# Kernel optimization log

Hardware: AMD Instinct MI355X
Metric: run time of the kernel (lower is better)

The kernel has to match this reference:

```python
import jax, jax.numpy as jnp
import numpy as np

DIMS = [2048, 1024, 512, 256, 128, 64, 32, 16, 8, 4, 2]
IN_CH = [3, 8, 32, 64, 64, 64, 128, 256, 512, 512, 512]
FEAT = [8, 32, 64, 64, 64, 128, 256, 512, 512, 512, 1024]
B = 512
K = 16


def setup_inputs() -> dict:
    key = jax.random.key(0)
    keys = jax.random.split(key, 64)
    inp = {"x": jax.random.normal(keys[0], (B, 3, 2048), dtype=jnp.float32)}
    for i, d in enumerate(DIMS):
        inp[f"c{i}"] = jax.random.randint(keys[1 + i], (d,), 0, 3, dtype=jnp.int64)
    for i in range(11):
        cin, f = IN_CH[i], FEAT[i]
        inp[f"W{i+1}"] = jax.random.normal(keys[20 + 2 * i], (3 * f, cin), dtype=jnp.float32) / jnp.sqrt(jnp.float32(cin))
        inp[f"b{i+1}"] = jnp.zeros((3 * f,), dtype=jnp.float32)
    inp["Wfc"] = jax.random.normal(keys[60], (K, 1024), dtype=jnp.float32) / jnp.sqrt(jnp.float32(1024))
    inp["bfc"] = jnp.zeros((K,), dtype=jnp.float32)
    return inp


def _kdconv(x, W, b, sel, featdim, dim):
    # pointwise conv (kernel size 1) + relu: [B, in, dim] -> [B, 3*featdim, dim]
    y = jax.nn.relu(jnp.einsum('oi,bid->bod', W, x) + b[None, :, None])
    bsz = y.shape[0]
    # faithful to torch: view [B, featdim, 3*dim], then gather index d*3 + sel[d]
    y = y.reshape(bsz, featdim, 3 * dim)
    idx = sel + 3 * jnp.arange(dim, dtype=sel.dtype)
    y = jnp.take(y, idx, axis=2)                       # [B, featdim, dim]
    y = y.reshape(bsz, featdim, dim // 2, 2)
    return jnp.max(y, axis=-1)                          # [B, featdim, dim//2]


def reference(x, c0, c1, c2, c3, c4, c5, c6, c7, c8, c9, c10,
              W1, b1, W2, b2, W3, b3, W4, b4, W5, b5, W6, b6,
              W7, b7, W8, b8, W9, b9, W10, b10, W11, b11, Wfc, bfc):
    cs = [c0, c1, c2, c3, c4, c5, c6, c7, c8, c9, c10]
    Ws = [W1, W2, W3, W4, W5, W6, W7, W8, W9, W10, W11]
    bs = [b1, b2, b3, b4, b5, b6, b7, b8, b9, b10, b11]
    y = x
    for i in range(11):
        y = _kdconv(y, Ws[i], bs[i], cs[i], FEAT[i], DIMS[i])
    y = y.reshape(-1, 1024)
    logits = y @ Wfc.T + bfc
    return jax.nn.log_softmax(logits, axis=1)
```

## Files before the change

### kernel.cpp

```cpp
#include <hip/hip_runtime.h>
#include <cstdint>
#include <cmath>


typedef __attribute__((ext_vector_type(8))) short bhalf8;
typedef __attribute__((ext_vector_type(4))) float floatx4;

__device__ __forceinline__ unsigned short f2bf(float f) {
    uint32_t u = __float_as_uint(f);
    u += 0x7FFFu + ((u >> 16) & 1u);
    return (unsigned short)(u >> 16);
}
__device__ __forceinline__ float bf2f(unsigned short u) {
    return __uint_as_float(((uint32_t)u) << 16);
}

struct WPrep {
    const float* src[9];
    unsigned short* dst[9];
    int n4[9];
};

__global__ __launch_bounds__(256)
void l01_kernel(const float* __restrict__ x,
                const float* __restrict__ W0, const float* __restrict__ b0,
                const int* __restrict__ sel0,
                const float* __restrict__ W1, const float* __restrict__ b1,
                const int* __restrict__ sel1,
                unsigned short* __restrict__ out,
                WPrep wp, int nL1) {
    const int tid = threadIdx.x;

    if ((int)blockIdx.x >= nL1) {
        const int stride = (gridDim.x - nL1) * 256;
        const int g0 = (blockIdx.x - nL1) * 256 + tid;
        #pragma unroll
        for (int l = 0; l < 9; ++l) {
            const float4* s = reinterpret_cast<const float4*>(wp.src[l]);
            uint2* d = reinterpret_cast<uint2*>(wp.dst[l]);
            for (int i = g0; i < wp.n4[l]; i += stride) {
                const float4 v = s[i];
                uint2 o;
                o.x = (uint32_t)f2bf(v.x) | ((uint32_t)f2bf(v.y) << 16);
                o.y = (uint32_t)f2bf(v.z) | ((uint32_t)f2bf(v.w) << 16);
                d[i] = o;
            }
        }
        return;
    }

    __shared__ float W0s[24][3]; __shared__ float b0s[24];
    __shared__ float W1s[96][8]; __shared__ float b1s[96];
    if (tid < 24) {
        W0s[tid][0] = W0[tid * 3 + 0];
        W0s[tid][1] = W0[tid * 3 + 1];
        W0s[tid][2] = W0[tid * 3 + 2];
        b0s[tid] = b0[tid];
    }
    if (tid < 96) {
        #pragma unroll
        for (int k = 0; k < 8; ++k) W1s[tid][k] = W1[tid * 8 + k];
        b1s[tid] = b1[tid];
    }
    __syncthreads();

    const int gid = blockIdx.x * 256 + tid;
    const int b  = gid >> 9;
    const int j1 = gid & 511;
    const float* xb = x + (size_t)b * 3 * 2048;

    float cols[2][8];
    int q1v[2];
    #pragma unroll
    for (int pos1 = 0; pos1 < 2; ++pos1) {
        const int d1 = 2 * j1 + pos1;
        const int e1 = 3 * d1 + sel1[d1];
        const int q1 = (e1 >= 1024) + (e1 >= 2048);
        const int p1 = e1 - q1 * 1024;
        q1v[pos1] = q1;

        float xv[2][3]; int qq0[2];
        #pragma unroll
        for (int pos0 = 0; pos0 < 2; ++pos0) {
            const int d0 = 2 * p1 + pos0;
            const int e0 = 3 * d0 + sel0[d0];
            const int q0 = (e0 >= 2048) + (e0 >= 4096);
            const int p0 = e0 - q0 * 2048;
            qq0[pos0] = q0;
            xv[pos0][0] = xb[p0];
            xv[pos0][1] = xb[2048 + p0];
            xv[pos0][2] = xb[4096 + p0];
        }
        #pragma unroll
        for (int f = 0; f < 8; ++f) {
            const int r0 = 3 * f + qq0[0], r1 = 3 * f + qq0[1];
            const float v0 = b0s[r0] + W0s[r0][0]*xv[0][0] + W0s[r0][1]*xv[0][1] + W0s[r0][2]*xv[0][2];
            const float v1 = b0s[r1] + W0s[r1][0]*xv[1][0] + W0s[r1][1]*xv[1][1] + W0s[r1][2]*xv[1][2];
            cols[pos1][f] = fmaxf(fmaxf(v0, v1), 0.f);
        }
    }

    unsigned short o[32];
    #pragma unroll
    for (int f = 0; f < 32; ++f) {
        const int r0 = 3 * f + q1v[0], r1 = 3 * f + q1v[1];
        float v0 = b1s[r0], v1 = b1s[r1];
        #pragma unroll
        for (int k = 0; k < 8; ++k) {
            v0 = fmaf(cols[0][k], W1s[r0][k], v0);
            v1 = fmaf(cols[1][k], W1s[r1][k], v1);
        }
        o[f] = f2bf(fmaxf(fmaxf(v0, v1), 0.f));
    }
    bhalf8* op = reinterpret_cast<bhalf8*>(out + (size_t)gid * 32);
    #pragma unroll
    for (int i = 0; i < 4; ++i) {
        bhalf8 v;
        #pragma unroll
        for (int k = 0; k < 8; ++k) v[k] = (short)o[8*i + k];
        op[i] = v;
    }
}


template<int RB>
__device__ __forceinline__ int swaddr(int row, int colbyte) {
    constexpr int SM = (RB / 16 >= 8) ? 7 : (RB / 16 - 1);
    return row * RB + (colbyte ^ ((row & SM) << 4));
}

template<int CIN>
__device__ __forceinline__ int wswz(int i) {
    constexpr int GPR = CIN / 8;
    constexpr int RB  = CIN * 2;
    const int row = i / GPR, c = i - row * GPR;
    return swaddr<RB>(row, c * 16);
}

template<int DIM, int CIN, int FEAT>
__device__ __forceinline__ void kdlayer(char* pool, int offIn, int offOut,
                                        int qpOff, int offW,
                                        const float* __restrict__ bg, int tid) {
    constexpr int NH  = CIN / 32;
    constexpr int MT  = DIM / 16;
    constexpr int NT  = FEAT / 16;
    constexpr int RBW = CIN * 2;
    constexpr int RBO = FEAT * 2;
    constexpr int WM  = (MT < 8) ? MT : 8;
    constexpr int WN  = 8 / WM;
    constexpr int MPW = MT / WM;
    constexpr int NPW = NT / WN;

    const unsigned short* qp = (const unsigned short*)(pool + qpOff);
    const int wv = tid >> 6, ln = tid & 63;
    const int g = ln >> 4, l15 = ln & 15;
    const int wm = wv % WM, wn = wv / WM;

    bhalf8 aC[MPW][NH];
    uint32_t qpk[MPW];
    #pragma unroll
    for (int i = 0; i < MPW; ++i) {
        const int mt = wm + i * WM;
        const int pa = qp[mt * 16 + l15] & 0xFFF;
        #pragma unroll
        for (int ks = 0; ks < NH; ++ks)
            aC[i][ks] = *(const bhalf8*)(pool + offIn +
                          swaddr<RBW>(pa, (ks * 32 + g * 8) * 2));
        const ushort4 qq = *(const ushort4*)(qp + mt * 16 + g * 4);
        qpk[i] = (uint32_t)(qq.x >> 12) | ((uint32_t)(qq.y >> 12) << 4)
               | ((uint32_t)(qq.z >> 12) << 8) | ((uint32_t)(qq.w >> 12) << 12);
    }

    #pragma unroll
    for (int ntj = 0; ntj < NPW; ++ntj) {
        const int nt = wn * NPW + ntj;
        const int f = nt * 16 + l15;
        bhalf8 bF[3][NH];
        #pragma unroll
        for (int q = 0; q < 3; ++q)
            #pragma unroll
            for (int ks = 0; ks < NH; ++ks)
                bF[q][ks] = *(const bhalf8*)(pool + offW +
                              swaddr<RBW>(3 * f + q, (ks * 32 + g * 8) * 2));
        const float bv0 = bg[3 * f + 0];
        const float bv1 = bg[3 * f + 1];
        const float bv2 = bg[3 * f + 2];
        #pragma unroll
        for (int i = 0; i < MPW; ++i) {
            floatx4 a0 = (floatx4){0.f,0.f,0.f,0.f};
            floatx4 a1 = (floatx4){0.f,0.f,0.f,0.f};
            floatx4 a2 = (floatx4){0.f,0.f,0.f,0.f};
            #pragma unroll
            for (int ks = 0; ks < NH; ++ks) {
                a0 = __builtin_amdgcn_mfma_f32_16x16x32_bf16(aC[i][ks], bF[0][ks], a0, 0, 0, 0);
                a1 = __builtin_amdgcn_mfma_f32_16x16x32_bf16(aC[i][ks], bF[1][ks], a1, 0, 0, 0);
                a2 = __builtin_amdgcn_mfma_f32_16x16x32_bf16(aC[i][ks], bF[2][ks], a2, 0, 0, 0);
            }
            const int mt = wm + i * WM;
            const int j0 = mt * 8 + g * 2;
            float v[4];
            #pragma unroll
            for (int r = 0; r < 4; ++r) {
                const int qi = (qpk[i] >> (4 * r)) & 0xF;
                const float pre = (qi == 0) ? a0[r] : (qi == 1 ? a1[r] : a2[r]);
                const float bq  = (qi == 0) ? bv0  : (qi == 1 ? bv1  : bv2);
                v[r] = pre + bq;
            }
            *(unsigned short*)(pool + offOut + swaddr<RBO>(j0,     f * 2)) =
                f2bf(fmaxf(fmaxf(v[0], v[1]), 0.f));
            *(unsigned short*)(pool + offOut + swaddr<RBO>(j0 + 1, f * 2)) =
                f2bf(fmaxf(fmaxf(v[2], v[3]), 0.f));
        }
    }
}

__global__ __launch_bounds__(512, 4)
void chain_kernel(const unsigned short* __restrict__ act,
                  unsigned short* __restrict__ out,
                  const unsigned short* __restrict__ w2, const float* __restrict__ b2, const int* __restrict__ s2,
                  const unsigned short* __restrict__ w3, const float* __restrict__ b3, const int* __restrict__ s3,
                  const unsigned short* __restrict__ w4, const float* __restrict__ b4, const int* __restrict__ s4,
                  const unsigned short* __restrict__ w5, const float* __restrict__ b5, const int* __restrict__ s5) {
    __shared__ __align__(16) char pool[79872];
    const int tid = threadIdx.x;
    const int b = blockIdx.x;

    bhalf8 w3r[3];
    #pragma unroll
    for (int u = 0; u < 3; ++u)
        w3r[u] = ((const bhalf8*)w3)[u * 512 + tid];

    {
        unsigned short* qp2 = (unsigned short*)(pool + 0);
        unsigned short* qp3 = (unsigned short*)(pool + 1024);
        unsigned short* qp4 = (unsigned short*)(pool + 1536);
        unsigned short* qp5 = (unsigned short*)(pool + 1792);
        { const int d = tid;
          const int e = 3 * d + s2[d];
          const int q = (e >= 512) + (e >= 1024);
          qp2[d] = (unsigned short)((q << 12) | (e - q * 512)); }
        if (tid < 256) { const int d = tid;
          const int e = 3 * d + s3[d];
          const int q = (e >= 256) + (e >= 512);
          qp3[d] = (unsigned short)((q << 12) | (e - q * 256)); }
        if (tid < 128) { const int d = tid;
          const int e = 3 * d + s4[d];
          const int q = (e >= 128) + (e >= 256);
          qp4[d] = (unsigned short)((q << 12) | (e - q * 128)); }
        if (tid < 64)  { const int d = tid;
          const int e = 3 * d + s5[d];
          const int q = (e >= 64) + (e >= 128);
          qp5[d] = (unsigned short)((q << 12) | (e - q * 64)); }
    }

    {
        const bhalf8* src = (const bhalf8*)(act + (size_t)b * 512 * 32);
        bhalf8 inr[4];
        #pragma unroll
        for (int k = 0; k < 4; ++k) inr[k] = src[k * 512 + tid];
        const bhalf8* ws = (const bhalf8*)w2;
        bhalf8 w2r[2];
        w2r[0] = ws[tid];
        if (tid < 256) w2r[1] = ws[512 + tid];
        #pragma unroll
        for (int k = 0; k < 4; ++k)
            *(bhalf8*)(pool + 2048 + wswz<32>(k * 512 + tid)) = inr[k];
        *(bhalf8*)(pool + 34816 + wswz<32>(tid)) = w2r[0];
        if (tid < 256)
            *(bhalf8*)(pool + 34816 + wswz<32>(512 + tid)) = w2r[1];
    }
    __syncthreads();

    kdlayer<512, 32, 64>(pool, 2048, 47104, 0, 34816, b2, tid);
    __syncthreads();

    bhalf8 w4r[3];
    #pragma unroll
    for (int u = 0; u < 3; ++u)
        w4r[u] = ((const bhalf8*)w4)[u * 512 + tid];
    #pragma unroll
    for (int u = 0; u < 3; ++u)
        *(bhalf8*)(pool + 2048 + wswz<64>(u * 512 + tid)) = w3r[u];
    __syncthreads();

    kdlayer<256, 64, 64>(pool, 47104, 26624, 1024, 2048, b3, tid);
    __syncthreads();

    bhalf8 w5r[6];
    #pragma unroll
    for (int u = 0; u < 6; ++u)
        w5r[u] = ((const bhalf8*)w5)[u * 512 + tid];
    #pragma unroll
    for (int u = 0; u < 3; ++u)
        *(bhalf8*)(pool + 47104 + wswz<64>(u * 512 + tid)) = w4r[u];
    __syncthreads();

    kdlayer<128, 64, 64>(pool, 26624, 71680, 1536, 47104, b4, tid);
    __syncthreads();

    #pragma unroll
    for (int u = 0; u < 6; ++u)
        *(bhalf8*)(pool + 2048 + wswz<64>(u * 512 + tid)) = w5r[u];
    __syncthreads();

    kdlayer<64, 64, 128>(pool, 71680, 51200, 1792, 2048, b5, tid);
    __syncthreads();

    {
        char* dst = (char*)(out + (size_t)b * 32 * 128);
        const int off = tid * 16;
        const bhalf8 v = *(const bhalf8*)(pool + 51200 +
                                          swaddr<256>(off >> 8, off & 255));
        *(bhalf8*)(dst + off) = v;
    }
}

template<int CIN, int BT>
__global__ __launch_bounds__(256)
void kdmfma_kernel(const unsigned short* __restrict__ act,
                   const unsigned short* __restrict__ Wq,
                   const float* __restrict__ bias,
                   const int*   __restrict__ sel,
                   unsigned short* __restrict__ out,
                   int feat, int dim, int nbt) {
    constexpr int KS  = (CIN >= 128) ? 128 : CIN;
    constexpr int NH  = KS / 32;
    constexpr int LDK = KS + 8;
    constexpr int TPA = 256 / BT;
    constexpr int EA  = KS / TPA;
    constexpr int NSA = EA / 8;
    constexpr int NSW = KS / 32;
    constexpr int MF  = 2;
    constexpr int NF  = (BT == 64) ? 2 : 1;
    __shared__ __align__(16) unsigned short Ab[BT][LDK];
    __shared__ __align__(16) unsigned short Wb[64][LDK];

    const int dimh = dim >> 1;
    const int bt = blockIdx.x % nbt;
    const int j  = blockIdx.x / nbt;
    const int f0 = blockIdx.y * 64;
    const int b0 = bt * BT;

    const int tid  = threadIdx.x;
    const int lane = tid & 63;
    const int wave = tid >> 6;

    const int srowA = tid / TPA;
    const int kgA   = (tid % TPA) * EA;
    const int srowW = tid >> 2;
    const int kgW   = (tid & 3) * (KS / 4);

    const int rowBase = (BT == 64) ? (wave & 1) * 32 : 0;
    const int colBase = (BT == 64) ? (wave >> 1) * 32 : wave * 16;

    floatx4 acc[2][MF][NF];
    #pragma unroll
    for (int pp = 0; pp < 2; ++pp)
        #pragma unroll
        for (int mi = 0; mi < MF; ++mi)
            #pragma unroll
            for (int ni = 0; ni < NF; ++ni)
                acc[pp][mi][ni] = (floatx4){0.f, 0.f, 0.f, 0.f};
    int qv[2];

    #pragma unroll
    for (int pp = 0; pp < 2; ++pp) {
        const int d = 2 * j + pp;
        const int s = sel[d];
        const int e = 3 * d + s;
        const int q = (e >= dim) + (e >= 2 * dim);
        const int p = e - q * dim;
        qv[pp] = q;

        const unsigned short* Ap = act + ((size_t)(b0 + srowA) * dim + p) * CIN + kgA;
        const unsigned short* Wp = Wq + ((size_t)(3 * (f0 + srowW) + q)) * CIN + kgW;

        bhalf8 pa[NSA], pw[NSW];
        #pragma unroll
        for (int u = 0; u < NSA; ++u)
            pa[u] = *reinterpret_cast<const bhalf8*>(Ap + u * 8);
        #pragma unroll
        for (int u = 0; u < NSW; ++u)
            pw[u] = *reinterpret_cast<const bhalf8*>(Wp + u * 8);

        for (int k0 = 0; k0 < CIN; k0 += KS) {
            __syncthreads();
            #pragma unroll
            for (int u = 0; u < NSA; ++u)
                *reinterpret_cast<bhalf8*>(&Ab[srowA][kgA + u * 8]) = pa[u];
            #pragma unroll
            for (int u = 0; u < NSW; ++u)
                *reinterpret_cast<bhalf8*>(&Wb[srowW][kgW + u * 8]) = pw[u];
            if (k0 + KS < CIN) {
                #pragma unroll
                for (int u = 0; u < NSA; ++u)
                    pa[u] = *reinterpret_cast<const bhalf8*>(Ap + k0 + KS + u * 8);
                #pragma unroll
                for (int u = 0; u < NSW; ++u)
                    pw[u] = *reinterpret_cast<const bhalf8*>(Wp + k0 + KS + u * 8);
            }
            __syncthreads();

            #pragma unroll
            for (int ks = 0; ks < NH; ++ks) {
                const int kk = ks * 32 + (lane >> 4) * 8;
                bhalf8 aF[MF], bF[NF];
                #pragma unroll
                for (int mi = 0; mi < MF; ++mi)
                    aF[mi] = *reinterpret_cast<const bhalf8*>(
                        &Ab[rowBase + mi * 16 + (lane & 15)][kk]);
                #pragma unroll
                for (int ni = 0; ni < NF; ++ni)
                    bF[ni] = *reinterpret_cast<const bhalf8*>(
                        &Wb[colBase + ni * 16 + (lane & 15)][kk]);
                #pragma unroll
                for (int mi = 0; mi < MF; ++mi)
                    #pragma unroll
                    for (int ni = 0; ni < NF; ++ni)
                        acc[pp][mi][ni] = __builtin_amdgcn_mfma_f32_16x16x32_bf16(
                            aF[mi], bF[ni], acc[pp][mi][ni], 0, 0, 0);
            }
        }
    }

    const int orow = (lane >> 4) << 2;
    const int ocol = lane & 15;
    #pragma unroll
    for (int mi = 0; mi < MF; ++mi)
        #pragma unroll
        for (int ni = 0; ni < NF; ++ni) {
            const int fc = f0 + colBase + ni * 16 + ocol;
            const float bv0 = bias[3 * fc + qv[0]];
            const float bv1 = bias[3 * fc + qv[1]];
            #pragma unroll
            for (int i = 0; i < 4; ++i) {
                const int br = b0 + rowBase + mi * 16 + orow + i;
                const float v = fmaxf(fmaxf(acc[0][mi][ni][i] + bv0,
                                            acc[1][mi][ni][i] + bv1), 0.f);
                out[((size_t)br * dimh + j) * feat + fc] = f2bf(v);
            }
        }
}

__global__ __launch_bounds__(256)
void fc_lsm_kernel(const unsigned short* __restrict__ y,
                   const float* __restrict__ Wfc,
                   const float* __restrict__ bfc,
                   float* __restrict__ out) {
    const int b   = blockIdx.x;
    const int tid = threadIdx.x;
    __shared__ __align__(16) float ys[1024];
    __shared__ float lg[16];

    {
        const ushort4 v = reinterpret_cast<const ushort4*>(y + (size_t)b * 1024)[tid];
        ys[tid * 4 + 0] = bf2f(v.x);
        ys[tid * 4 + 1] = bf2f(v.y);
        ys[tid * 4 + 2] = bf2f(v.z);
        ys[tid * 4 + 3] = bf2f(v.w);
    }
    __syncthreads();

    const int l = tid >> 4, lane = tid & 15;
    const float4* w4 = reinterpret_cast<const float4*>(Wfc + (size_t)l * 1024);
    const float4* y4 = reinterpret_cast<const float4*>(ys);
    float p = 0.f;
    #pragma unroll
    for (int i = 0; i < 16; ++i) {
        const float4 a = y4[lane + 16 * i];
        const float4 w = w4[lane + 16 * i];
        p += a.x * w.x + a.y * w.y + a.z * w.z + a.w * w.w;
    }
    #pragma unroll
    for (int off = 8; off > 0; off >>= 1) p += __shfl_down(p, off, 16);
    if (lane == 0) lg[l] = p + bfc[l];
    __syncthreads();

    if (tid < 16) {
        float m = -1e30f;
        #pragma unroll
        for (int i = 0; i < 16; ++i) m = fmaxf(m, lg[i]);
        float s = 0.f;
        #pragma unroll
        for (int i = 0; i < 16; ++i) s += expf(lg[i] - m);
        out[b * 16 + tid] = lg[tid] - m - logf(s);
    }
}

extern "C" void kernel_launch(void* const* d_in, const int* in_sizes, int n_in,
                              void* d_out, int out_size, void* d_ws, size_t ws_size,
                              hipStream_t stream) {
    static const int LFEAT[11] = {8, 32, 64, 64, 64, 128, 256, 512, 512, 512, 1024};
    static const int LDIM[11]  = {2048, 1024, 512, 256, 128, 64, 32, 16, 8, 4, 2};
    static const int LCIN[11]  = {3, 8, 32, 64, 64, 64, 128, 256, 512, 512, 512};

    const float* x = (const float*)d_in[0];
    const int B = in_sizes[0] / (3 * 2048);

    const size_t slot = (size_t)B * 32 * 512;
    float* bufA = (float*)d_ws;
    float* bufB = bufA + slot;
    unsigned short* wq = (unsigned short*)(bufB + slot);

    const float* W[11]; const float* bi[11]; const int* sl[11];
    for (int i = 0; i < 11; ++i) {
        W[i]  = (const float*)d_in[12 + 2 * i];
        bi[i] = (const float*)d_in[13 + 2 * i];
        sl[i] = (const int*)d_in[1 + i];
    }

    unsigned short* wqp[11];
    {
        size_t off = 0;
        for (int i = 2; i <= 10; ++i) {
            wqp[i] = wq + off;
            off += (size_t)3 * LFEAT[i] * LCIN[i];
        }
    }

    unsigned short* actA = (unsigned short*)bufA;
    unsigned short* actB = (unsigned short*)bufB;

    {
        WPrep wp;
        for (int i = 2; i <= 10; ++i) {
            wp.src[i - 2] = W[i];
            wp.dst[i - 2] = wqp[i];
            wp.n4[i - 2]  = (3 * LFEAT[i] * LCIN[i]) / 4;
        }
        const int nL1 = (B * 512) / 256;
        l01_kernel<<<nL1 + 768, 256, 0, stream>>>(x, W[0], bi[0], sl[0],
                                                  W[1], bi[1], sl[1],
                                                  actB, wp, nL1);
    }

    chain_kernel<<<B, 512, 0, stream>>>(actB, actA,
                                        wqp[2], bi[2], sl[2],
                                        wqp[3], bi[3], sl[3],
                                        wqp[4], bi[4], sl[4],
                                        wqp[5], bi[5], sl[5]);

    const int nbt64 = B / 64;
    const int nbt32 = B / 32;

    {   dim3 g((LDIM[6]/2) * nbt64, LFEAT[6]/64);
        kdmfma_kernel<128, 64><<<g, 256, 0, stream>>>(actA, wqp[6], bi[6], sl[6], actB, LFEAT[6], LDIM[6], nbt64); }
    {   dim3 g((LDIM[7]/2) * nbt64, LFEAT[7]/64);
        kdmfma_kernel<256, 64><<<g, 256, 0, stream>>>(actB, wqp[7], bi[7], sl[7], actA, LFEAT[7], LDIM[7], nbt64); }

    {   dim3 g((LDIM[8]/2) * nbt32, LFEAT[8]/64);
        kdmfma_kernel<512, 32><<<g, 256, 0, stream>>>(actA, wqp[8], bi[8], sl[8], actB, LFEAT[8], LDIM[8], nbt32); }
    {   dim3 g((LDIM[9]/2) * nbt32, LFEAT[9]/64);
        kdmfma_kernel<512, 32><<<g, 256, 0, stream>>>(actB, wqp[9], bi[9], sl[9], actA, LFEAT[9], LDIM[9], nbt32); }
    {   dim3 g((LDIM[10]/2) * nbt32, LFEAT[10]/64);
        kdmfma_kernel<512, 32><<<g, 256, 0, stream>>>(actA, wqp[10], bi[10], sl[10], actB, LFEAT[10], LDIM[10], nbt32); }

    fc_lsm_kernel<<<B, 256, 0, stream>>>(actB, (const float*)d_in[34],
                                         (const float*)d_in[35], (float*)d_out);
}
```

Before: 85.29 us.

## Fuse layers 0-1 into chain kernel, split weight prep, add kdmfma2 for deep layers

Layers 0 and 1 are now computed inside chain_kernel, which writes their output straight into shared memory. This removes the global round-trip of the layer-1 activations and one kernel launch. Weight conversion to bf16 is split in two. A small kernel converts the layer 2-5 weights up front, and extra blocks appended to chain_kernel convert the layer 6-10 weights while the chain runs. Layers 8-10 switch to a new MFMA kernel with a fixed 128-wide K step and register-prefetched double staging. Risks include extra register pressure in chain_kernel and changed tile efficiency for the deep layers.

```diff
diff --git a/kernel.cpp b/kernel.cpp
--- a/kernel.cpp
+++ b/kernel.cpp
@@ -16,109 +16,26 @@
 }
 
 struct WPrep {
-    const float* src[9];
-    unsigned short* dst[9];
-    int n4[9];
+    const float* src[5];
+    unsigned short* dst[5];
+    int n4[5];
 };
 
 __global__ __launch_bounds__(256)
-void l01_kernel(const float* __restrict__ x,
-                const float* __restrict__ W0, const float* __restrict__ b0,
-                const int* __restrict__ sel0,
-                const float* __restrict__ W1, const float* __restrict__ b1,
-                const int* __restrict__ sel1,
-                unsigned short* __restrict__ out,
-                WPrep wp, int nL1) {
-    const int tid = threadIdx.x;
-
-    if ((int)blockIdx.x >= nL1) {
-        const int stride = (gridDim.x - nL1) * 256;
-        const int g0 = (blockIdx.x - nL1) * 256 + tid;
-        #pragma unroll
-        for (int l = 0; l < 9; ++l) {
-            const float4* s = reinterpret_cast<const float4*>(wp.src[l]);
-            uint2* d = reinterpret_cast<uint2*>(wp.dst[l]);
-            for (int i = g0; i < wp.n4[l]; i += stride) {
-                const float4 v = s[i];
-                uint2 o;
-                o.x = (uint32_t)f2bf(v.x) | ((uint32_t)f2bf(v.y) << 16);
-                o.y = (uint32_t)f2bf(v.z) | ((uint32_t)f2bf(v.w) << 16);
-                d[i] = o;
-            }
-        }
-        return;
-    }
-
-    __shared__ float W0s[24][3]; __shared__ float b0s[24];
-    __shared__ float W1s[96][8]; __shared__ float b1s[96];
-    if (tid < 24) {
-        W0s[tid][0] = W0[tid * 3 + 0];
-        W0s[tid][1] = W0[tid * 3 + 1];
-        W0s[tid][2] = W0[tid * 3 + 2];
-        b0s[tid] = b0[tid];
-    }
-    if (tid < 96) {
-        #pragma unroll
-        for (int k = 0; k < 8; ++k) W1s[tid][k] = W1[tid * 8 + k];
-        b1s[tid] = b1[tid];
-    }
-    __syncthreads();
-
-    const int gid = blockIdx.x * 256 + tid;
-    const int b  = gid >> 9;
-    const int j1 = gid & 511;
-    const float* xb = x + (size_t)b * 3 * 2048;
-
-    float cols[2][8];
-    int q1v[2];
-    #pragma unroll
-    for (int pos1 = 0; pos1 < 2; ++pos1) {
-        const int d1 = 2 * j1 + pos1;
-        const int e1 = 3 * d1 + sel1[d1];
-        const int q1 = (e1 >= 1024) + (e1 >= 2048);
-        const int p1 = e1 - q1 * 1024;
-        q1v[pos1] = q1;
-
-        float xv[2][3]; int qq0[2];
-        #pragma unroll
-        for (int pos0 = 0; pos0 < 2; ++pos0) {
-            const int d0 = 2 * p1 + pos0;
-            const int e0 = 3 * d0 + sel0[d0];
-            const int q0 = (e0 >= 2048) + (e0 >= 4096);
-            const int p0 = e0 - q0 * 2048;
-            qq0[pos0] = q0;
-            xv[pos0][0] = xb[p0];
-            xv[pos0][1] = xb[2048 + p0];
-            xv[pos0][2] = xb[4096 + p0];
-        }
-        #pragma unroll
-        for (int f = 0; f < 8; ++f) {
-            const int r0 = 3 * f + qq0[0], r1 = 3 * f + qq0[1];
-            const float v0 = b0s[r0] + W0s[r0][0]*xv[0][0] + W0s[r0][1]*xv[0][1] + W0s[r0][2]*xv[0][2];
-            const float v1 = b0s[r1] + W0s[r1][0]*xv[1][0] + W0s[r1][1]*xv[1][1] + W0s[r1][2]*xv[1][2];
-            cols[pos1][f] = fmaxf(fmaxf(v0, v1), 0.f);
-        }
-    }
-
-    unsigned short o[32];
-    #pragma unroll
-    for (int f = 0; f < 32; ++f) {
-        const int r0 = 3 * f + q1v[0], r1 = 3 * f + q1v[1];
-        float v0 = b1s[r0], v1 = b1s[r1];
-        #pragma unroll
-        for (int k = 0; k < 8; ++k) {
-            v0 = fmaf(cols[0][k], W1s[r0][k], v0);
-            v1 = fmaf(cols[1][k], W1s[r1][k], v1);
-        }
-        o[f] = f2bf(fmaxf(fmaxf(v0, v1), 0.f));
-    }
-    bhalf8* op = reinterpret_cast<bhalf8*>(out + (size_t)gid * 32);
-    #pragma unroll
-    for (int i = 0; i < 4; ++i) {
-        bhalf8 v;
-        #pragma unroll
-        for (int k = 0; k < 8; ++k) v[k] = (short)o[8*i + k];
-        op[i] = v;
+void wprep25_kernel(WPrep wp) {
+    const int stride = gridDim.x * 256;
+    const int g0 = blockIdx.x * 256 + threadIdx.x;
+    #pragma unroll
+    for (int l = 0; l < 4; ++l) {
+        const float4* s = reinterpret_cast<const float4*>(wp.src[l]);
+        uint2* d = reinterpret_cast<uint2*>(wp.dst[l]);
+        for (int i = g0; i < wp.n4[l]; i += stride) {
+            const float4 v = s[i];
+            uint2 o;
+            o.x = (uint32_t)f2bf(v.x) | ((uint32_t)f2bf(v.y) << 16);
+            o.y = (uint32_t)f2bf(v.z) | ((uint32_t)f2bf(v.w) << 16);
+            d[i] = o;
+        }
     }
 }
 
@@ -215,21 +132,63 @@
 }
 
 __global__ __launch_bounds__(512, 4)
-void chain_kernel(const unsigned short* __restrict__ act,
-                  unsigned short* __restrict__ out,
+void chain_kernel(const float* __restrict__ x,
+                  const float* __restrict__ W0, const float* __restrict__ b0f,
+                  const int* __restrict__ sel0,
+                  const float* __restrict__ W1, const float* __restrict__ b1f,
+                  const int* __restrict__ sel1,
+                  unsigned short* __restrict__ outp,
                   const unsigned short* __restrict__ w2, const float* __restrict__ b2, const int* __restrict__ s2,
                   const unsigned short* __restrict__ w3, const float* __restrict__ b3, const int* __restrict__ s3,
                   const unsigned short* __restrict__ w4, const float* __restrict__ b4, const int* __restrict__ s4,
-                  const unsigned short* __restrict__ w5, const float* __restrict__ b5, const int* __restrict__ s5) {
+                  const unsigned short* __restrict__ w5, const float* __restrict__ b5, const int* __restrict__ s5,
+                  WPrep wp, int nrows) {
+    const int tid = threadIdx.x;
+
+    if ((int)blockIdx.x >= nrows) {
+        const int stride = (gridDim.x - nrows) * 512;
+        const int g0 = (blockIdx.x - nrows) * 512 + tid;
+        #pragma unroll
+        for (int l = 0; l < 5; ++l) {
+            const float4* s = reinterpret_cast<const float4*>(wp.src[l]);
+            uint2* d = reinterpret_cast<uint2*>(wp.dst[l]);
+            for (int i = g0; i < wp.n4[l]; i += stride) {
+                const float4 v = s[i];
+                uint2 o;
+                o.x = (uint32_t)f2bf(v.x) | ((uint32_t)f2bf(v.y) << 16);
+                o.y = (uint32_t)f2bf(v.z) | ((uint32_t)f2bf(v.w) << 16);
+                d[i] = o;
+            }
+        }
+        return;
+    }
+
     __shared__ __align__(16) char pool[79872];
-    const int tid = threadIdx.x;
     const int b = blockIdx.x;
 
     bhalf8 w3r[3];
     #pragma unroll
     for (int u = 0; u < 3; ++u)
         w3r[u] = ((const bhalf8*)w3)[u * 512 + tid];
-
+    bhalf8 w2r[2];
+    w2r[0] = ((const bhalf8*)w2)[tid];
+    if (tid < 256) w2r[1] = ((const bhalf8*)w2)[512 + tid];
+
+    float* W0s = (float*)(pool + 47104);
+    float* b0s = W0s + 72;
+    float* W1s = b0s + 24;
+    float* b1s = W1s + 768;
+    if (tid < 24) {
+        W0s[tid * 3 + 0] = W0[tid * 3 + 0];
+        W0s[tid * 3 + 1] = W0[tid * 3 + 1];
+        W0s[tid * 3 + 2] = W0[tid * 3 + 2];
+        b0s[tid] = b0f[tid];
+    }
+    if (tid < 96) {
+        #pragma unroll
+        for (int k = 0; k < 8; ++k) W1s[tid * 8 + k] = W1[tid * 8 + k];
+        b1s[tid] = b1f[tid];
+    }
     {
         unsigned short* qp2 = (unsigned short*)(pool + 0);
         unsigned short* qp3 = (unsigned short*)(pool + 1024);
@@ -252,23 +211,63 @@
           const int q = (e >= 64) + (e >= 128);
           qp5[d] = (unsigned short)((q << 12) | (e - q * 64)); }
     }
+    __syncthreads();
 
     {
-        const bhalf8* src = (const bhalf8*)(act + (size_t)b * 512 * 32);
-        bhalf8 inr[4];
-        #pragma unroll
-        for (int k = 0; k < 4; ++k) inr[k] = src[k * 512 + tid];
-        const bhalf8* ws = (const bhalf8*)w2;
-        bhalf8 w2r[2];
-        w2r[0] = ws[tid];
-        if (tid < 256) w2r[1] = ws[512 + tid];
-        #pragma unroll
-        for (int k = 0; k < 4; ++k)
-            *(bhalf8*)(pool + 2048 + wswz<32>(k * 512 + tid)) = inr[k];
-        *(bhalf8*)(pool + 34816 + wswz<32>(tid)) = w2r[0];
-        if (tid < 256)
-            *(bhalf8*)(pool + 34816 + wswz<32>(512 + tid)) = w2r[1];
-    }
+        const int j1 = tid;
+        const float* xb = x + (size_t)b * 3 * 2048;
+
+        float cols[2][8];
+        int q1v[2];
+        #pragma unroll
+        for (int pos1 = 0; pos1 < 2; ++pos1) {
+            const int d1 = 2 * j1 + pos1;
+            const int e1 = 3 * d1 + sel1[d1];
+            const int q1 = (e1 >= 1024) + (e1 >= 2048);
+            const int p1 = e1 - q1 * 1024;
+            q1v[pos1] = q1;
+
+            float xv[2][3]; int qq0[2];
+            #pragma unroll
+            for (int pos0 = 0; pos0 < 2; ++pos0) {
+                const int d0 = 2 * p1 + pos0;
+                const int e0 = 3 * d0 + sel0[d0];
+                const int q0 = (e0 >= 2048) + (e0 >= 4096);
+                const int p0 = e0 - q0 * 2048;
+                qq0[pos0] = q0;
+                xv[pos0][0] = xb[p0];
+                xv[pos0][1] = xb[2048 + p0];
+                xv[pos0][2] = xb[4096 + p0];
+            }
+            #pragma unroll
+            for (int f = 0; f < 8; ++f) {
+                const int r0 = 3 * f + qq0[0], r1 = 3 * f + qq0[1];
+                const float v0 = b0s[r0] + W0s[r0*3+0]*xv[0][0] + W0s[r0*3+1]*xv[0][1] + W0s[r0*3+2]*xv[0][2];
+                const float v1 = b0s[r1] + W0s[r1*3+0]*xv[1][0] + W0s[r1*3+1]*xv[1][1] + W0s[r1*3+2]*xv[1][2];
+                cols[pos1][f] = fmaxf(fmaxf(v0, v1), 0.f);
+            }
+        }
+        #pragma unroll
+        for (int gi = 0; gi < 4; ++gi) {
+            bhalf8 og;
+            #pragma unroll
+            for (int fk = 0; fk < 8; ++fk) {
+                const int f = gi * 8 + fk;
+                const int r0 = 3 * f + q1v[0], r1 = 3 * f + q1v[1];
+                float v0 = b1s[r0], v1 = b1s[r1];
+                #pragma unroll
+                for (int k = 0; k < 8; ++k) {
+                    v0 = fmaf(cols[0][k], W1s[r0*8+k], v0);
+                    v1 = fmaf(cols[1][k], W1s[r1*8+k], v1);
+                }
+                og[fk] = (short)f2bf(fmaxf(fmaxf(v0, v1), 0.f));
+            }
+            *(bhalf8*)(pool + 2048 + swaddr<64>(j1, gi * 16)) = og;
+        }
+    }
+    *(bhalf8*)(pool + 34816 + wswz<32>(tid)) = w2r[0];
+    if (tid < 256)
+        *(bhalf8*)(pool + 34816 + wswz<32>(512 + tid)) = w2r[1];
     __syncthreads();
 
     kdlayer<512, 32, 64>(pool, 2048, 47104, 0, 34816, b2, tid);
@@ -307,7 +306,7 @@
     __syncthreads();
 
     {
-        char* dst = (char*)(out + (size_t)b * 32 * 128);
+        char* dst = (char*)(outp + (size_t)b * 32 * 128);
         const int off = tid * 16;
         const bhalf8 v = *(const bhalf8*)(pool + 51200 +
                                           swaddr<256>(off >> 8, off & 255));
@@ -442,6 +441,136 @@
         }
 }
 
+template<int CIN, int BT>
+__global__ __launch_bounds__(256)
+void kdmfma2_kernel(const unsigned short* __restrict__ act,
+                    const unsigned short* __restrict__ Wq,
+                    const float* __restrict__ bias,
+                    const int*   __restrict__ sel,
+                    unsigned short* __restrict__ out,
+                    int feat, int dim, int nbt) {
+    constexpr int KS  = 128;
+    constexpr int NH  = KS / 32;
+    constexpr int LDK = KS + 8;
+    constexpr int TPA = 256 / BT;
+    constexpr int EA  = KS / TPA;
+    constexpr int NSA = EA / 8;
+    constexpr int NSW = KS / 32;
+    constexpr int MF  = 2;
+    __shared__ __align__(16) unsigned short Ab[2][BT][LDK];
+    __shared__ __align__(16) unsigned short Wb[2][64][LDK];
+
+    const int dimh = dim >> 1;
+    const int bt = blockIdx.x % nbt;
+    const int j  = blockIdx.x / nbt;
+    const int f0 = blockIdx.y * 64;
+    const int b0 = bt * BT;
+
+    const int tid  = threadIdx.x;
+    const int lane = tid & 63;
+    const int wave = tid >> 6;
+
+    const int srowA = tid / TPA;
+    const int kgA   = (tid % TPA) * EA;
+    const int srowW = tid >> 2;
+    const int kgW   = (tid & 3) * (KS / 4);
+    const int colBase = wave * 16;
+
+    int qv[2];
+    const unsigned short* Ap[2];
+    const unsigned short* Wp[2];
+    #pragma unroll
+    for (int pp = 0; pp < 2; ++pp) {
+        const int d = 2 * j + pp;
+        const int e = 3 * d + sel[d];
+        const int q = (e >= dim) + (e >= 2 * dim);
+        const int p = e - q * dim;
+        qv[pp] = q;
+        Ap[pp] = act + ((size_t)(b0 + srowA) * dim + p) * CIN + kgA;
+        Wp[pp] = Wq + ((size_t)(3 * (f0 + srowW) + q)) * CIN + kgW;
+    }
+
+    floatx4 acc[2][MF];
+    #pragma unroll
+    for (int pp = 0; pp < 2; ++pp)
+        #pragma unroll
+        for (int mi = 0; mi < MF; ++mi)
+            acc[pp][mi] = (floatx4){0.f, 0.f, 0.f, 0.f};
+
+    bhalf8 pa[2][NSA], pw[2][NSW];
+    #pragma unroll
+    for (int pp = 0; pp < 2; ++pp) {
+        #pragma unroll
+        for (int u = 0; u < NSA; ++u)
+            pa[pp][u] = *reinterpret_cast<const bhalf8*>(Ap[pp] + u * 8);
+        #pragma unroll
+        for (int u = 0; u < NSW; ++u)
+            pw[pp][u] = *reinterpret_cast<const bhalf8*>(Wp[pp] + u * 8);
+    }
+
+    for (int k0 = 0; k0 < CIN; k0 += KS) {
+        __syncthreads();
+        #pragma unroll
+        for (int pp = 0; pp < 2; ++pp) {
+            #pragma unroll
+            for (int u = 0; u < NSA; ++u)
+                *reinterpret_cast<bhalf8*>(&Ab[pp][srowA][kgA + u * 8]) = pa[pp][u];
+            #pragma unroll
+            for (int u = 0; u < NSW; ++u)
+                *reinterpret_cast<bhalf8*>(&Wb[pp][srowW][kgW + u * 8]) = pw[pp][u];
+        }
+        if (k0 + KS < CIN) {
+            #pragma unroll
+            for (int pp = 0; pp < 2; ++pp) {
+                #pragma unroll
+                for (int u = 0; u < NSA; ++u)
+                    pa[pp][u] = *reinterpret_cast<const bhalf8*>(Ap[pp] + k0 + KS + u * 8);
+                #pragma unroll
+                for (int u = 0; u < NSW; ++u)
+                    pw[pp][u] = *reinterpret_cast<const bhalf8*>(Wp[pp] + k0 + KS + u * 8);
+            }
+        }
+        __syncthreads();
+
+        #pragma unroll
+        for (int ks = 0; ks < NH; ++ks) {
+            const int kk = ks * 32 + (lane >> 4) * 8;
+            bhalf8 aF[2][MF], bF[2];
+            #pragma unroll
+            for (int pp = 0; pp < 2; ++pp) {
+                #pragma unroll
+                for (int mi = 0; mi < MF; ++mi)
+                    aF[pp][mi] = *reinterpret_cast<const bhalf8*>(
+                        &Ab[pp][mi * 16 + (lane & 15)][kk]);
+                bF[pp] = *reinterpret_cast<const bhalf8*>(
+                        &Wb[pp][colBase + (lane & 15)][kk]);
+            }
+            #pragma unroll
+            for (int pp = 0; pp < 2; ++pp)
+                #pragma unroll
+                for (int mi = 0; mi < MF; ++mi)
+                    acc[pp][mi] = __builtin_amdgcn_mfma_f32_16x16x32_bf16(
+                        aF[pp][mi], bF[pp], acc[pp][mi], 0, 0, 0);
+        }
+    }
+
+    const int orow = (lane >> 4) << 2;
+    const int ocol = lane & 15;
+    #pragma unroll
+    for (int mi = 0; mi < MF; ++mi) {
+        const int fc = f0 + colBase + ocol;
+        const float bv0 = bias[3 * fc + qv[0]];
+        const float bv1 = bias[3 * fc + qv[1]];
+        #pragma unroll
+        for (int i = 0; i < 4; ++i) {
+            const int br = b0 + mi * 16 + orow + i;
+            const float v = fmaxf(fmaxf(acc[0][mi][i] + bv0,
+                                        acc[1][mi][i] + bv1), 0.f);
+            out[((size_t)br * dimh + j) * feat + fc] = f2bf(v);
+        }
+    }
+}
+
 __global__ __launch_bounds__(256)
 void fc_lsm_kernel(const unsigned short* __restrict__ y,
                    const float* __restrict__ Wfc,
@@ -523,22 +652,28 @@
 
     {
         WPrep wp;
-        for (int i = 2; i <= 10; ++i) {
+        for (int i = 2; i <= 5; ++i) {
             wp.src[i - 2] = W[i];
             wp.dst[i - 2] = wqp[i];
             wp.n4[i - 2]  = (3 * LFEAT[i] * LCIN[i]) / 4;
         }
-        const int nL1 = (B * 512) / 256;
-        l01_kernel<<<nL1 + 768, 256, 0, stream>>>(x, W[0], bi[0], sl[0],
-                                                  W[1], bi[1], sl[1],
-                                                  actB, wp, nL1);
-    }
-
-    chain_kernel<<<B, 512, 0, stream>>>(actB, actA,
-                                        wqp[2], bi[2], sl[2],
-                                        wqp[3], bi[3], sl[3],
-                                        wqp[4], bi[4], sl[4],
-                                        wqp[5], bi[5], sl[5]);
+        wp.src[4] = nullptr; wp.dst[4] = nullptr; wp.n4[4] = 0;
+        wprep25_kernel<<<64, 256, 0, stream>>>(wp);
+    }
+
+    {
+        WPrep wp;
+        for (int i = 6; i <= 10; ++i) {
+            wp.src[i - 6] = W[i];
+            wp.dst[i - 6] = wqp[i];
+            wp.n4[i - 6]  = (3 * LFEAT[i] * LCIN[i]) / 4;
+        }
+        chain_kernel<<<B + 256, 512, 0, stream>>>(
+            x, W[0], bi[0], sl[0], W[1], bi[1], sl[1], actA,
+            wqp[2], bi[2], sl[2], wqp[3], bi[3], sl[3],
+            wqp[4], bi[4], sl[4], wqp[5], bi[5], sl[5],
+            wp, B);
+    }
 
     const int nbt64 = B / 64;
     const int nbt32 = B / 32;
@@ -549,11 +684,11 @@
         kdmfma_kernel<256, 64><<<g, 256, 0, stream>>>(actB, wqp[7], bi[7], sl[7], actA, LFEAT[7], LDIM[7], nbt64); }
 
     {   dim3 g((LDIM[8]/2) * nbt32, LFEAT[8]/64);
-        kdmfma_kernel<512, 32><<<g, 256, 0, stream>>>(actA, wqp[8], bi[8], sl[8], actB, LFEAT[8], LDIM[8], nbt32); }
+        kdmfma2_kernel<512, 32><<<g, 256, 0, stream>>>(actA, wqp[8], bi[8], sl[8], actB, LFEAT[8], LDIM[8], nbt32); }
     {   dim3 g((LDIM[9]/2) * nbt32, LFEAT[9]/64);
-        kdmfma_kernel<512, 32><<<g, 256, 0, stream>>>(actB, wqp[9], bi[9], sl[9], actA, LFEAT[9], LDIM[9], nbt32); }
+        kdmfma2_kernel<512, 32><<<g, 256, 0, stream>>>(actB, wqp[9], bi[9], sl[9], actA, LFEAT[9], LDIM[9], nbt32); }
     {   dim3 g((LDIM[10]/2) * nbt32, LFEAT[10]/64);
-        kdmfma_kernel<512, 32><<<g, 256, 0, stream>>>(actA, wqp[10], bi[10], sl[10], actB, LFEAT[10], LDIM[10], nbt32); }
+        kdmfma2_kernel<512, 32><<<g, 256, 0, stream>>>(actA, wqp[10], bi[10], sl[10], actB, LFEAT[10], LDIM[10], nbt32); }
 
     fc_lsm_kernel<<<B, 256, 0, stream>>>(actB, (const float*)d_in[34],
                                          (const float*)d_in[35], (float*)d_out);
```

Result: faster. 82.31 us (-3.5%).
